# Optimization experiments

Hardware: AMD Instinct MI355X
Metric: run time of the kernel (lower is better)

The kernel has to match this reference:

```python
import jax, jax.numpy as jnp
import numpy as np

B, S = 128, 256
BERT_DIM, HID, LATENT = 768, 512, 128
V = 4096        # size of valid-token id universe (valid_ids_set ~= arange(V))
K = 100         # n_clusters
VOCAB = 30522   # bow.shape[1]


def setup_inputs() -> dict:
    key = jax.random.key(0)
    ks = jax.random.split(key, 16)
    f = jnp.float32
    s = 0.02
    return {
        "input_ids": jax.random.randint(ks[0], (B, S), 0, V),
        "valid_pos": jnp.ones((B, S), jnp.int32),
        "attention_mask": jnp.ones((B, S), jnp.int32),
        "token_embs": jax.random.normal(ks[1], (B, S, BERT_DIM), f),
        "bow": jax.random.randint(ks[2], (B, VOCAB), 0, 2).astype(f),
        "enc_w1": jax.random.normal(ks[3], (BERT_DIM, HID), f) * s,
        "enc_b1": jnp.zeros((HID,), f),
        "enc_w2": jax.random.normal(ks[4], (HID, LATENT), f) * s,
        "enc_b2": jnp.zeros((LATENT,), f),
        "dec_w1": jax.random.normal(ks[5], (LATENT, HID), f) * s,
        "dec_b1": jnp.zeros((HID,), f),
        "dec_w2": jax.random.normal(ks[6], (HID, BERT_DIM), f) * s,
        "dec_b2": jnp.zeros((BERT_DIM,), f),
        "centers": jax.random.normal(ks[7], (K, LATENT), f),
        "counts": jnp.full((K,), 50.0, f),
        "vocab_weights": jax.random.uniform(ks[8], (VOCAB,), f),
    }


def reference(input_ids, valid_pos, attention_mask, token_embs, bow,
              enc_w1, enc_b1, enc_w2, enc_b2,
              dec_w1, dec_b1, dec_w2, dec_b2,
              centers, counts, vocab_weights):
    # valid_pos is all-ones -> valid_mask selects every token; flatten [B,S,D] -> [N,D]
    x = token_embs.reshape(-1, BERT_DIM)
    # AutoEncoder: encode, L2-normalize latent, decode
    h = jax.nn.relu(x @ enc_w1 + enc_b1)
    z = h @ enc_w2 + enc_b2
    z = z / jnp.linalg.norm(z, axis=-1, keepdims=True)          # latent_embs [N,LATENT]
    rec = jax.nn.relu(z @ dec_w1 + dec_b1) @ dec_w2 + dec_b2    # bert_embs_rec [N,768]
    # segment mean over unique token ids (valid_ids_set == arange(V))
    ids = input_ids.reshape(-1)
    seg_sum = jax.ops.segment_sum(z, ids, num_segments=V)
    freq = jax.ops.segment_sum(jnp.ones_like(ids, jnp.float32), ids, num_segments=V)
    avg = seg_sum / jnp.maximum(freq, 1.0)[:, None]             # avg_latent_embs [V,LATENT]
    # co-occurrence matrix: trans_matrix gathers bow columns at valid ids (= first V cols)
    nz = (bow[:, :V] != 0).astype(jnp.float32)                  # [B,V]
    p_i = nz.sum(axis=0) / B
    p_ij = (nz.T @ nz) / B                                      # [V,V]
    co_matrix = p_ij / p_i[:, None] / p_i[None, :]
    # soft k-means assignment: normalized centers, matmul, softmax, argmax
    cn = centers / jnp.linalg.norm(centers, axis=-1, keepdims=True)
    probs = jax.nn.softmax(avg @ cn.T, axis=-1)                 # [V,K]
    cluster_ids = jnp.argmax(probs, axis=1)
    # sequential EMA centroid update (equivalent ordering to per-cluster python loops;
    # clusters are independent so a single scan in sample order matches the original)
    w = vocab_weights[:V]
    valid = (freq > 0).astype(jnp.float32)                      # skip ids never seen

    def step(carry, inp):
        c, cnt = carry
        xi, ki, wi, vi = inp
        new_cnt = cnt[ki] + vi
        cnt = cnt.at[ki].set(new_cnt)
        eta = jnp.where(vi > 0, wi / new_cnt, 0.0)
        c = c.at[ki].set((1.0 - eta) * c[ki] + eta * xi)
        return (c, cnt), None

    (new_centers, _), _ = jax.lax.scan(step, (centers, counts), (avg, cluster_ids, w, valid))
    return co_matrix, rec, avg, cluster_ids, new_centers
```

## Files before the change

### kernel.cpp

```cpp
#include <hip/hip_runtime.h>
#include <cstdint>

#define M_TOK 32768
#define BERT  768
#define HID   512
#define LAT   128
#define NV    4096
#define NK    100
#define VOCAB 30522
#define NB    128

typedef short short8 __attribute__((ext_vector_type(8)));
typedef float floatx4 __attribute__((ext_vector_type(4)));
typedef unsigned short u16x4 __attribute__((ext_vector_type(4)));

__device__ __forceinline__ unsigned short f2bf(float f) {
    unsigned u = __float_as_uint(f);
    unsigned r = (u + 0x7FFFu + ((u >> 16) & 1u)) >> 16;
    return (unsigned short)r;
}
__device__ __forceinline__ float bf2f(unsigned short h) {
    return __uint_as_float((unsigned)h << 16);
}

__device__ __forceinline__ void async16(const void* g, void* l) {
    __builtin_amdgcn_global_load_lds(
        (const __attribute__((address_space(1))) unsigned int*)g,
        (__attribute__((address_space(3))) unsigned int*)l, 16, 0, 0);
}

__global__ __launch_bounds__(256) void wsplit(
    const float* __restrict__ W, unsigned short* __restrict__ Wt,
    int K, int N)
{
    int j = blockIdx.x * 256 + threadIdx.x;
    int total = N * K;
    if (j >= total) return;
    int n = j / K, k = j - n * K;
    float v = W[(size_t)k * N + n];
    unsigned short h = f2bf(v);
    float r = v - bf2f(h);
    unsigned short m = f2bf(r);
    float r2 = r - bf2f(m);
    unsigned short l = f2bf(r2);
    Wt[j] = h;
    Wt[(size_t)total + j] = m;
    Wt[(size_t)2 * total + j] = l;
}

__global__ __launch_bounds__(256) void asplit(
    const float* __restrict__ A, unsigned short* __restrict__ P, int total)
{
    int j = (blockIdx.x * 256 + threadIdx.x) * 4;
    if (j >= total) return;
    float4 v4 = *(const float4*)(A + j);
    float vv[4] = {v4.x, v4.y, v4.z, v4.w};
    u16x4 h4, m4, l4;
#pragma unroll
    for (int e = 0; e < 4; ++e) {
        float v = vv[e];
        unsigned short h = f2bf(v);
        float r = v - bf2f(h);
        unsigned short m = f2bf(r);
        float r2 = r - bf2f(m);
        h4[e] = h; m4[e] = m; l4[e] = f2bf(r2);
    }
    *(u16x4*)(P + j) = h4;
    *(u16x4*)(P + (size_t)total + j) = m4;
    *(u16x4*)(P + (size_t)2 * total + j) = l4;
}

template<int NL, bool RELU, int OUT = 0>
__global__ __launch_bounds__(256) void gemm_mfma(
    const float* __restrict__ A, const unsigned short* __restrict__ Wt,
    const float* __restrict__ bias, float* __restrict__ C,
    int M, int N, int K)
{
    __shared__ unsigned short Ash[NL][128 * 32];
    __shared__ unsigned short Bsh[NL][128 * 32];

    const int tid  = threadIdx.x;
    const int lane = tid & 63;
    const int wave = tid >> 6;
    const int bm = blockIdx.y * 128;
    const int bn = blockIdx.x * 128;
    const int wm = (wave & 1) * 64;
    const int wn = (wave >> 1) * 64;

    const int ar = tid >> 3;
    const int ak = (tid & 7) * 4;
    const int br = tid >> 2;
    const int bk = (tid & 3) * 8;

    floatx4 acc[4][4];
#pragma unroll
    for (int t = 0; t < 4; ++t)
#pragma unroll
        for (int u = 0; u < 4; ++u)
            acc[t][u] = (floatx4)0.0f;

    float4 av[4];
#pragma unroll
    for (int i = 0; i < 4; ++i)
        av[i] = *(const float4*)(A + (size_t)(bm + ar + 32 * i) * K + ak);

    for (int k0 = 0; k0 < K; k0 += 32) {
        u16x4 ah[NL][4];
#pragma unroll
        for (int i = 0; i < 4; ++i) {
            float vv[4] = {av[i].x, av[i].y, av[i].z, av[i].w};
#pragma unroll
            for (int e = 0; e < 4; ++e) {
                float v = vv[e];
                unsigned short h = f2bf(v);
                float r = v - bf2f(h);
                unsigned short m = f2bf(r);
                ah[0][i][e] = h;
                ah[1][i][e] = m;
                if (NL == 3) {
                    float r2 = r - bf2f(m);
                    ah[2][i][e] = f2bf(r2);
                }
            }
        }
        __syncthreads();
#pragma unroll
        for (int l = 0; l < NL; ++l) {
            const unsigned short* wp = Wt + (size_t)l * N * K;
#pragma unroll
            for (int i = 0; i < 2; ++i)
                async16(wp + (size_t)(bn + br + 64 * i) * K + k0 + bk,
                        &Bsh[l][i * 2048 + tid * 8]);
        }
#pragma unroll
        for (int l = 0; l < NL; ++l)
#pragma unroll
            for (int i = 0; i < 4; ++i)
                *(u16x4*)&Ash[l][(ar + 32 * i) * 32 + ak] = ah[l][i];
        if (k0 + 32 < K) {
#pragma unroll
            for (int i = 0; i < 4; ++i)
                av[i] = *(const float4*)(A + (size_t)(bm + ar + 32 * i) * K + k0 + 32 + ak);
        }
        __syncthreads();

        short8 af[NL][4];
#pragma unroll
        for (int l = 0; l < NL; ++l)
#pragma unroll
            for (int t = 0; t < 4; ++t)
                af[l][t] = *(const short8*)&Ash[l][(wm + t * 16 + (lane & 15)) * 32 + (lane >> 4) * 8];

#pragma unroll
        for (int bl = 0; bl < NL; ++bl) {
            short8 bf[4];
#pragma unroll
            for (int u = 0; u < 4; ++u)
                bf[u] = *(const short8*)&Bsh[bl][(wn + u * 16 + (lane & 15)) * 32 + (lane >> 4) * 8];
#pragma unroll
            for (int al = 0; al < NL; ++al) {
                if (al + bl >= NL) continue;
#pragma unroll
                for (int t = 0; t < 4; ++t)
#pragma unroll
                    for (int u = 0; u < 4; ++u)
                        acc[t][u] = __builtin_amdgcn_mfma_f32_16x16x32_bf16(
                            af[al][t], bf[u], acc[t][u], 0, 0, 0);
            }
        }
    }

    unsigned short* P0 = (unsigned short*)C;
    unsigned short* P1 = P0 + (size_t)M * N;
#pragma unroll
    for (int t = 0; t < 4; ++t) {
        int row0 = bm + wm + t * 16 + (lane >> 4) * 4;
#pragma unroll
        for (int u = 0; u < 4; ++u) {
            int col = bn + wn + u * 16 + (lane & 15);
            float b = bias[col];
#pragma unroll
            for (int r = 0; r < 4; ++r) {
                float v = acc[t][u][r] + b;
                if (RELU) v = fmaxf(v, 0.f);
                if (OUT == 0) {
                    C[(size_t)(row0 + r) * N + col] = v;
                } else {
                    unsigned short hh = f2bf(v);
                    unsigned short mm = f2bf(v - bf2f(hh));
                    P0[(size_t)(row0 + r) * N + col] = hh;
                    P1[(size_t)(row0 + r) * N + col] = mm;
                }
            }
        }
    }
}

template<int NP, bool RELU>
__global__ __launch_bounds__(512, 2) void gemm8p(
    const unsigned short* __restrict__ Ap,
    const unsigned short* __restrict__ Bp,
    const float* __restrict__ bias, float* __restrict__ C,
    int M, int N, int K, int NT)
{
    __shared__ unsigned short As[2][256 * 64];
    __shared__ unsigned short Bs[2][256 * 64];

    const int tid  = threadIdx.x;
    const int lane = tid & 63;
    const int wid  = tid >> 6;
    const int wm   = (wid & 1) * 128;
    const int wn   = (wid >> 1) * 64;
    const int bm   = blockIdx.y * 256;
    const int bn   = blockIdx.x * 256;

    const int laneR = lane & 15;
    const int kgrp  = lane >> 4;
    const int swz   = lane & 7;
    const int slot0 = ((kgrp)     ^ swz) * 8;
    const int slot1 = ((4 + kgrp) ^ swz) * 8;
    const int abase = (wm + laneR) * 64;
    const int bbase = (wn + laneR) * 64;

    floatx4 acc[8][4];
#pragma unroll
    for (int m = 0; m < 8; ++m)
#pragma unroll
        for (int n = 0; n < 4; ++n) acc[m][n] = (floatx4)0.0f;

    auto stage = [&](int b, int T) {
        int c0 = 2 * T, c1 = 2 * T + 1;
        int ki0, j0, ki1, j1, al0, bl0, al1, bl1;
        if (NP == 6) {
            ki0 = c0 / 6; j0 = c0 - ki0 * 6;
            ki1 = c1 / 6; j1 = c1 - ki1 * 6;
            al0 = j0 < 3 ? j0 : (j0 < 5 ? j0 - 3 : 0);
            bl0 = j0 < 3 ? 0  : (j0 < 5 ? 1 : 2);
            al1 = j1 < 3 ? j1 : (j1 < 5 ? j1 - 3 : 0);
            bl1 = j1 < 3 ? 0  : (j1 < 5 ? 1 : 2);
        } else {
            ki0 = c0 / 3; j0 = c0 - ki0 * 3;
            ki1 = c1 / 3; j1 = c1 - ki1 * 3;
            al0 = (j0 == 1); bl0 = (j0 == 2);
            al1 = (j1 == 1); bl1 = (j1 == 2);
        }
        const unsigned short* A0 = Ap + (size_t)al0 * M * K + ki0 * 32;
        const unsigned short* A1 = Ap + (size_t)al1 * M * K + ki1 * 32;
        const unsigned short* B0 = Bp + (size_t)bl0 * N * K + ki0 * 32;
        const unsigned short* B1 = Bp + (size_t)bl1 * N * K + ki1 * 32;
#pragma unroll
        for (int i = 0; i < 4; ++i) {
            int s   = i * 512 + tid;
            int row = s >> 3;
            int e0  = ((s & 7) ^ (row & 7)) * 8;
            const unsigned short* src = ((e0 & 32) ? A1 : A0)
                                        + (size_t)(bm + row) * K + (e0 & 31);
            async16(src, &As[b][s * 8]);
        }
#pragma unroll
        for (int i = 0; i < 4; ++i) {
            int s   = i * 512 + tid;
            int row = s >> 3;
            int e0  = ((s & 7) ^ (row & 7)) * 8;
            const unsigned short* src = ((e0 & 32) ? B1 : B0)
                                        + (size_t)(bn + row) * K + (e0 & 31);
            async16(src, &Bs[b][s * 8]);
        }
    };

    stage(0, 0);
    stage(1, 1);

    for (int t = 0; t < NT; ++t) {
        const int cb = t & 1;
        if (t + 1 < NT) asm volatile("s_waitcnt vmcnt(8)" ::: "memory");
        else            asm volatile("s_waitcnt vmcnt(0)" ::: "memory");
        __builtin_amdgcn_s_barrier();
        asm volatile("" ::: "memory");

        const unsigned short* Ab = &As[cb][0];
        const unsigned short* Bb = &Bs[cb][0];
        short8 a0[4][2], a1[4][2], b0f[2][2], b1f[2][2];
#pragma unroll
        for (int m = 0; m < 4; ++m) {
            a0[m][0] = *(const short8*)&Ab[abase + m * 1024 + slot0];
            a0[m][1] = *(const short8*)&Ab[abase + m * 1024 + slot1];
        }
        __builtin_amdgcn_sched_barrier(0);
#pragma unroll
        for (int n = 0; n < 2; ++n) {
            b0f[n][0] = *(const short8*)&Bb[bbase + n * 1024 + slot0];
            b0f[n][1] = *(const short8*)&Bb[bbase + n * 1024 + slot1];
        }
        __builtin_amdgcn_sched_barrier(0);
#pragma unroll
        for (int n = 0; n < 2; ++n) {
            b1f[n][0] = *(const short8*)&Bb[bbase + (2 + n) * 1024 + slot0];
            b1f[n][1] = *(const short8*)&Bb[bbase + (2 + n) * 1024 + slot1];
        }
        __builtin_amdgcn_sched_barrier(0);
#pragma unroll
        for (int m = 0; m < 4; ++m) {
            a1[m][0] = *(const short8*)&Ab[abase + (4 + m) * 1024 + slot0];
            a1[m][1] = *(const short8*)&Ab[abase + (4 + m) * 1024 + slot1];
        }

        asm volatile("s_waitcnt lgkmcnt(12)" ::: "memory");
        __builtin_amdgcn_sched_barrier(0);
        __builtin_amdgcn_s_setprio(1);
#pragma unroll
        for (int m = 0; m < 4; ++m)
#pragma unroll
            for (int n = 0; n < 2; ++n)
#pragma unroll
                for (int kk = 0; kk < 2; ++kk)
                    acc[m][n] = __builtin_amdgcn_mfma_f32_16x16x32_bf16(
                        a0[m][kk], b0f[n][kk], acc[m][n], 0, 0, 0);
        __builtin_amdgcn_s_setprio(0);

        asm volatile("s_waitcnt lgkmcnt(8)" ::: "memory");
        __builtin_amdgcn_sched_barrier(0);
        __builtin_amdgcn_s_setprio(1);
#pragma unroll
        for (int m = 0; m < 4; ++m)
#pragma unroll
            for (int n = 0; n < 2; ++n)
#pragma unroll
                for (int kk = 0; kk < 2; ++kk)
                    acc[m][2 + n] = __builtin_amdgcn_mfma_f32_16x16x32_bf16(
                        a0[m][kk], b1f[n][kk], acc[m][2 + n], 0, 0, 0);
        __builtin_amdgcn_s_setprio(0);

        asm volatile("s_waitcnt lgkmcnt(0)" ::: "memory");
        __builtin_amdgcn_sched_barrier(0);
        asm volatile("" ::: "memory");
        __builtin_amdgcn_s_barrier();
        asm volatile("" ::: "memory");
        if (t + 2 < NT) stage(cb, t + 2);

        __builtin_amdgcn_s_setprio(1);
#pragma unroll
        for (int m = 0; m < 4; ++m)
#pragma unroll
            for (int n = 0; n < 2; ++n)
#pragma unroll
                for (int kk = 0; kk < 2; ++kk)
                    acc[4 + m][2 + n] = __builtin_amdgcn_mfma_f32_16x16x32_bf16(
                        a1[m][kk], b1f[n][kk], acc[4 + m][2 + n], 0, 0, 0);
#pragma unroll
        for (int m = 0; m < 4; ++m)
#pragma unroll
            for (int n = 0; n < 2; ++n)
#pragma unroll
                for (int kk = 0; kk < 2; ++kk)
                    acc[4 + m][n] = __builtin_amdgcn_mfma_f32_16x16x32_bf16(
                        a1[m][kk], b0f[n][kk], acc[4 + m][n], 0, 0, 0);
        __builtin_amdgcn_s_setprio(0);
    }

#pragma unroll
    for (int mf = 0; mf < 8; ++mf) {
        int row0 = bm + wm + mf * 16 + (lane >> 4) * 4;
#pragma unroll
        for (int nf = 0; nf < 4; ++nf) {
            int col = bn + wn + nf * 16 + (lane & 15);
            float b = bias[col];
#pragma unroll
            for (int r = 0; r < 4; ++r) {
                float v = acc[mf][nf][r] + b;
                if (RELU) v = fmaxf(v, 0.f);
                C[(size_t)(row0 + r) * N + col] = v;
            }
        }
    }
}

__global__ __launch_bounds__(64) void rownorm128(const float* __restrict__ in,
                                                 float* __restrict__ out)
{
    int row = blockIdx.x;
    int l = threadIdx.x;
    const float* p = in + (size_t)row * 128;
    float v0 = p[l], v1 = p[l + 64];
    float s = v0 * v0 + v1 * v1;
#pragma unroll
    for (int o = 32; o > 0; o >>= 1) s += __shfl_xor(s, o, 64);
    float inv = 1.0f / sqrtf(s);
    float* q = out + (size_t)row * 128;
    q[l] = v0 * inv;
    q[l + 64] = v1 * inv;
}

__global__ __launch_bounds__(128) void seg_scatter(
    const float* __restrict__ z, const int* __restrict__ ids,
    float* __restrict__ seg, float* __restrict__ freq)
{
    int row = blockIdx.x;
    int l = threadIdx.x;
    int id = ids[row];
    atomicAdd(&seg[(size_t)id * 128 + l], z[(size_t)row * 128 + l]);
    if (l == 0) atomicAdd(&freq[id], 1.0f);
}

__global__ __launch_bounds__(128) void avg_kernel(
    const float* __restrict__ seg, const float* __restrict__ freq,
    float* __restrict__ avg)
{
    int i = blockIdx.x;
    int l = threadIdx.x;
    float f = fmaxf(freq[i], 1.0f);
    avg[(size_t)i * 128 + l] = seg[(size_t)i * 128 + l] / f;
}

__global__ __launch_bounds__(128) void argmax_kernel(
    const float* __restrict__ avg, const float* __restrict__ cn,
    int* __restrict__ cids, float* __restrict__ cids_f)
{
    __shared__ float arow[128];
    __shared__ float lg[NK];
    int row = blockIdx.x;
    int t = threadIdx.x;
    arow[t] = avg[(size_t)row * 128 + t];
    __syncthreads();
    if (t < NK) {
        float d = 0.f;
        const float* c = cn + (size_t)t * 128;
#pragma unroll 8
        for (int i = 0; i < 128; ++i) d += arow[i] * c[i];
        lg[t] = d;
    }
    __syncthreads();
    if (t == 0) {
        float best = lg[0];
        int bi = 0;
        for (int k = 1; k < NK; ++k) {
            if (lg[k] > best) { best = lg[k]; bi = k; }
        }
        cids[row] = bi;
        cids_f[row] = (float)bi;
    }
}

__global__ __launch_bounds__(256) void build_masks(
    const float* __restrict__ bow, unsigned long long* __restrict__ masks,
    float* __restrict__ cnt)
{
    int j = blockIdx.x * 256 + threadIdx.x;
    if (j >= NV) return;
    unsigned long long m0 = 0, m1 = 0;
    for (int b = 0; b < 64; ++b)
        if (bow[(size_t)b * VOCAB + j] != 0.f) m0 |= 1ull << b;
    for (int b = 0; b < 64; ++b)
        if (bow[(size_t)(b + 64) * VOCAB + j] != 0.f) m1 |= 1ull << b;
    masks[2 * j] = m0;
    masks[2 * j + 1] = m1;
    cnt[j] = (float)(__popcll(m0) + __popcll(m1));
}

__global__ __launch_bounds__(256) void co_kernel(
    const unsigned long long* __restrict__ masks, const float* __restrict__ cnt,
    float* __restrict__ co)
{
    int j = blockIdx.x * 256 + threadIdx.x;
    unsigned long long m0 = masks[2 * j], m1 = masks[2 * j + 1];
    float cj = cnt[j];
    int ibase = blockIdx.y * 64;
    for (int ii = 0; ii < 64; ++ii) {
        int i = ibase + ii;
        unsigned long long a0 = masks[2 * i], a1 = masks[2 * i + 1];
        float ci = cnt[i];
        float c = (float)(__popcll(a0 & m0) + __popcll(a1 & m1));
        co[(size_t)i * NV + j] = (float)NB * c / (ci * cj);
    }
}

__global__ __launch_bounds__(128) void cluster_scan(
    const float* __restrict__ avg, const int* __restrict__ cids,
    const float* __restrict__ freq, const float* __restrict__ vw,
    const float* __restrict__ centers, const float* __restrict__ counts,
    float* __restrict__ out_centers)
{
    __shared__ int list[NV];
    __shared__ float coef[NV];
    __shared__ int tcnt[128];
    __shared__ int tot;
    __shared__ float Ptot;

    int k = blockIdx.x;
    int t = threadIdx.x;

    int base = t * (NV / 128);
    int c = 0;
    for (int s = 0; s < NV / 128; ++s) {
        int i = base + s;
        if (cids[i] == k && freq[i] > 0.f) c++;
    }
    tcnt[t] = c;
    __syncthreads();
    if (t == 0) {
        int run = 0;
        for (int x = 0; x < 128; ++x) { int v = tcnt[x]; tcnt[x] = run; run += v; }
        tot = run;
    }
    __syncthreads();
    int off = tcnt[t];
    for (int s = 0; s < NV / 128; ++s) {
        int i = base + s;
        if (cids[i] == k && freq[i] > 0.f) list[off++] = i;
    }
    __syncthreads();
    int m = tot;

    float c0 = counts[k];
    for (int j = t; j < m; j += 128)
        coef[j] = vw[list[j]] / (c0 + (float)(j + 1));
    __syncthreads();
    if (t == 0) {
        float suf = 1.f;
        for (int j = m - 1; j >= 0; --j) {
            float e = coef[j];
            coef[j] = e * suf;
            suf *= (1.f - e);
        }
        Ptot = suf;
    }
    __syncthreads();

    float accv = Ptot * centers[(size_t)k * 128 + t];
    for (int j = 0; j < m; ++j)
        accv += coef[j] * avg[(size_t)list[j] * 128 + t];
    out_centers[(size_t)k * 128 + t] = accv;
}

__global__ __launch_bounds__(64) void cn_norm(const float* __restrict__ centers,
                                              float* __restrict__ cn)
{
    int row = blockIdx.x;
    int l = threadIdx.x;
    const float* p = centers + (size_t)row * 128;
    float v0 = p[l], v1 = p[l + 64];
    float s = v0 * v0 + v1 * v1;
#pragma unroll
    for (int o = 32; o > 0; o >>= 1) s += __shfl_xor(s, o, 64);
    float inv = 1.0f / sqrtf(s);
    cn[(size_t)row * 128 + l] = v0 * inv;
    cn[(size_t)row * 128 + l + 64] = v1 * inv;
}

extern "C" void kernel_launch(void* const* d_in, const int* in_sizes, int n_in,
                              void* d_out, int out_size, void* d_ws, size_t ws_size,
                              hipStream_t stream)
{
    const int*   input_ids = (const int*)d_in[0];
    const float* token_embs = (const float*)d_in[3];
    const float* bow       = (const float*)d_in[4];
    const float* enc_w1    = (const float*)d_in[5];
    const float* enc_b1    = (const float*)d_in[6];
    const float* enc_w2    = (const float*)d_in[7];
    const float* enc_b2    = (const float*)d_in[8];
    const float* dec_w1    = (const float*)d_in[9];
    const float* dec_b1    = (const float*)d_in[10];
    const float* dec_w2    = (const float*)d_in[11];
    const float* dec_b2    = (const float*)d_in[12];
    const float* centers   = (const float*)d_in[13];
    const float* counts    = (const float*)d_in[14];
    const float* vocab_w   = (const float*)d_in[15];

    float* out = (float*)d_out;
    const size_t OFF_CO  = 0;
    const size_t OFF_REC = 16777216;
    const size_t OFF_AVG = OFF_REC + 25165824;
    const size_t OFF_CID = OFF_AVG + 524288;
    const size_t OFF_NC  = OFF_CID + 4096;

    float* h    = (float*)d_ws;
    float* z    = h + (size_t)M_TOK * HID;
    float* seg  = z + (size_t)M_TOK * LAT;
    float* freq = seg + (size_t)NV * LAT;
    float* cn   = freq + NV;
    float* cntv = cn + (size_t)NK * LAT;
    int*   cids = (int*)(cntv + NV);
    unsigned long long* masks = (unsigned long long*)(cids + NV);
    unsigned short* wt1 = (unsigned short*)(masks + 2 * NV);
    unsigned short* wt2 = wt1 + (size_t)3 * HID * BERT;
    unsigned short* wt3 = wt2 + (size_t)3 * LAT * HID;
    unsigned short* wt4 = wt3 + (size_t)3 * HID * LAT;

    unsigned short* a1p = (unsigned short*)out;

    hipMemsetAsync(seg, 0, (size_t)(NV * LAT + NV) * sizeof(float), stream);

    wsplit<<<(BERT * HID + 255) / 256, 256, 0, stream>>>(enc_w1, wt1, BERT, HID);
    wsplit<<<(HID * LAT + 255) / 256, 256, 0, stream>>>(enc_w2, wt2, HID, LAT);
    wsplit<<<(LAT * HID + 255) / 256, 256, 0, stream>>>(dec_w1, wt3, LAT, HID);
    wsplit<<<(HID * BERT + 255) / 256, 256, 0, stream>>>(dec_w2, wt4, HID, BERT);

    asplit<<<(M_TOK * BERT / 4 + 255) / 256, 256, 0, stream>>>(
        token_embs, a1p, M_TOK * BERT);

    gemm8p<6, true><<<dim3(HID / 256, M_TOK / 256), 512, 0, stream>>>(
        a1p, wt1, enc_b1, h, M_TOK, HID, BERT, 6 * BERT / 64);

    gemm_mfma<3, false><<<dim3(LAT / 128, M_TOK / 128), 256, 0, stream>>>(
        h, wt2, enc_b2, z, M_TOK, LAT, HID);
    rownorm128<<<M_TOK, 64, 0, stream>>>(z, z);

    gemm_mfma<2, true, 2><<<dim3(HID / 128, M_TOK / 128), 256, 0, stream>>>(
        z, wt3, dec_b1, h, M_TOK, HID, LAT);

    gemm8p<3, false><<<dim3(BERT / 256, M_TOK / 256), 512, 0, stream>>>(
        (const unsigned short*)h, wt4, dec_b2, out + OFF_REC,
        M_TOK, BERT, HID, 3 * HID / 64);

    seg_scatter<<<M_TOK, 128, 0, stream>>>(z, input_ids, seg, freq);
    avg_kernel<<<NV, 128, 0, stream>>>(seg, freq, out + OFF_AVG);

    cn_norm<<<NK, 64, 0, stream>>>(centers, cn);
    argmax_kernel<<<NV, 128, 0, stream>>>(out + OFF_AVG, cn, cids, out + OFF_CID);

    build_masks<<<NV / 256, 256, 0, stream>>>(bow, masks, cntv);
    co_kernel<<<dim3(NV / 256, NV / 64), 256, 0, stream>>>(masks, cntv, out + OFF_CO);

    cluster_scan<<<NK, 128, 0, stream>>>(out + OFF_AVG, cids, freq, vocab_w,
                                         centers, counts, out + OFF_NC);
}
```

Before: 782.9 us.

## Split GEMM tile staging into half-tile loads interleaved with MFMA phases

```diff
diff --git a/kernel.cpp b/kernel.cpp
--- a/kernel.cpp
+++ b/kernel.cpp
@@ -228,84 +228,67 @@
 #pragma unroll
         for (int n = 0; n < 4; ++n) acc[m][n] = (floatx4)0.0f;
 
-    auto stage = [&](int b, int T) {
-        int c0 = 2 * T, c1 = 2 * T + 1;
-        int ki0, j0, ki1, j1, al0, bl0, al1, bl1;
+    auto decode = [&](int c, int& ki, int& al, int& bl) {
         if (NP == 6) {
-            ki0 = c0 / 6; j0 = c0 - ki0 * 6;
-            ki1 = c1 / 6; j1 = c1 - ki1 * 6;
-            al0 = j0 < 3 ? j0 : (j0 < 5 ? j0 - 3 : 0);
-            bl0 = j0 < 3 ? 0  : (j0 < 5 ? 1 : 2);
-            al1 = j1 < 3 ? j1 : (j1 < 5 ? j1 - 3 : 0);
-            bl1 = j1 < 3 ? 0  : (j1 < 5 ? 1 : 2);
+            ki = c / 6; int j = c - ki * 6;
+            al = j < 3 ? j : (j < 5 ? j - 3 : 0);
+            bl = j < 3 ? 0 : (j < 5 ? 1 : 2);
         } else {
-            ki0 = c0 / 3; j0 = c0 - ki0 * 3;
-            ki1 = c1 / 3; j1 = c1 - ki1 * 3;
-            al0 = (j0 == 1); bl0 = (j0 == 2);
-            al1 = (j1 == 1); bl1 = (j1 == 2);
-        }
-        const unsigned short* A0 = Ap + (size_t)al0 * M * K + ki0 * 32;
-        const unsigned short* A1 = Ap + (size_t)al1 * M * K + ki1 * 32;
-        const unsigned short* B0 = Bp + (size_t)bl0 * N * K + ki0 * 32;
-        const unsigned short* B1 = Bp + (size_t)bl1 * N * K + ki1 * 32;
-#pragma unroll
-        for (int i = 0; i < 4; ++i) {
-            int s   = i * 512 + tid;
-            int row = s >> 3;
-            int e0  = ((s & 7) ^ (row & 7)) * 8;
-            const unsigned short* src = ((e0 & 32) ? A1 : A0)
-                                        + (size_t)(bm + row) * K + (e0 & 31);
-            async16(src, &As[b][s * 8]);
-        }
-#pragma unroll
-        for (int i = 0; i < 4; ++i) {
-            int s   = i * 512 + tid;
-            int row = s >> 3;
-            int e0  = ((s & 7) ^ (row & 7)) * 8;
-            const unsigned short* src = ((e0 & 32) ? B1 : B0)
-                                        + (size_t)(bn + row) * K + (e0 & 31);
-            async16(src, &Bs[b][s * 8]);
+            ki = c / 3; int j = c - ki * 3;
+            al = (j == 1); bl = (j == 2);
         }
     };
 
-    stage(0, 0);
-    stage(1, 1);
+    auto stageH = [&](int mat, int half, int T) {
+        int ki0, al0, bl0, ki1, al1, bl1;
+        decode(2 * T, ki0, al0, bl0);
+        decode(2 * T + 1, ki1, al1, bl1);
+        const unsigned short *base0, *base1;
+        int bro;
+        unsigned short* dst;
+        if (mat == 0) {
+            base0 = Ap + (size_t)al0 * M * K + (size_t)ki0 * 32;
+            base1 = Ap + (size_t)al1 * M * K + (size_t)ki1 * 32;
+            bro = bm; dst = &As[T & 1][0];
+        } else {
+            base0 = Bp + (size_t)bl0 * N * K + (size_t)ki0 * 32;
+            base1 = Bp + (size_t)bl1 * N * K + (size_t)ki1 * 32;
+            bro = bn; dst = &Bs[T & 1][0];
+        }
+#pragma unroll
+        for (int i = 0; i < 2; ++i) {
+            int row = half * 128 + i * 64 + (tid >> 3);
+            int e0  = ((tid & 7) ^ (row & 7)) * 8;
+            const unsigned short* src = ((e0 & 32) ? base1 : base0)
+                                        + (size_t)(bro + row) * K + (e0 & 31);
+            async16(src, dst + row * 64 + (tid & 7) * 8);
+        }
+    };
+
+    stageH(1, 0, 0); stageH(0, 0, 0); stageH(1, 1, 0); stageH(0, 1, 0);
+    stageH(1, 0, 1); stageH(0, 0, 1);
+    asm volatile("s_waitcnt vmcnt(4)" ::: "memory");
+    __builtin_amdgcn_s_barrier();
 
     for (int t = 0; t < NT; ++t) {
         const int cb = t & 1;
-        if (t + 1 < NT) asm volatile("s_waitcnt vmcnt(8)" ::: "memory");
-        else            asm volatile("s_waitcnt vmcnt(0)" ::: "memory");
-        __builtin_amdgcn_s_barrier();
-        asm volatile("" ::: "memory");
-
         const unsigned short* Ab = &As[cb][0];
         const unsigned short* Bb = &Bs[cb][0];
-        short8 a0[4][2], a1[4][2], b0f[2][2], b1f[2][2];
+        short8 af[4][2], bl_[2][2], bh_[2][2];
+
 #pragma unroll
         for (int m = 0; m < 4; ++m) {
-            a0[m][0] = *(const short8*)&Ab[abase + m * 1024 + slot0];
-            a0[m][1] = *(const short8*)&Ab[abase + m * 1024 + slot1];
-        }
-        __builtin_amdgcn_sched_barrier(0);
+            af[m][0] = *(const short8*)&Ab[abase + m * 1024 + slot0];
+            af[m][1] = *(const short8*)&Ab[abase + m * 1024 + slot1];
+        }
 #pragma unroll
         for (int n = 0; n < 2; ++n) {
-            b0f[n][0] = *(const short8*)&Bb[bbase + n * 1024 + slot0];
-            b0f[n][1] = *(const short8*)&Bb[bbase + n * 1024 + slot1];
-        }
-        __builtin_amdgcn_sched_barrier(0);
-#pragma unroll
-        for (int n = 0; n < 2; ++n) {
-            b1f[n][0] = *(const short8*)&Bb[bbase + (2 + n) * 1024 + slot0];
-            b1f[n][1] = *(const short8*)&Bb[bbase + (2 + n) * 1024 + slot1];
-        }
-        __builtin_amdgcn_sched_barrier(0);
-#pragma unroll
-        for (int m = 0; m < 4; ++m) {
-            a1[m][0] = *(const short8*)&Ab[abase + (4 + m) * 1024 + slot0];
-            a1[m][1] = *(const short8*)&Ab[abase + (4 + m) * 1024 + slot1];
-        }
-
-        asm volatile("s_waitcnt lgkmcnt(12)" ::: "memory");
+            bl_[n][0] = *(const short8*)&Bb[bbase + n * 1024 + slot0];
+            bl_[n][1] = *(const short8*)&Bb[bbase + n * 1024 + slot1];
+        }
+        if (t + 1 < NT) stageH(1, 1, t + 1);
+        __builtin_amdgcn_s_barrier();
+        asm volatile("s_waitcnt lgkmcnt(0)" ::: "memory");
         __builtin_amdgcn_sched_barrier(0);
         __builtin_amdgcn_s_setprio(1);
 #pragma unroll
@@ -315,10 +298,18 @@
 #pragma unroll
                 for (int kk = 0; kk < 2; ++kk)
                     acc[m][n] = __builtin_amdgcn_mfma_f32_16x16x32_bf16(
-                        a0[m][kk], b0f[n][kk], acc[m][n], 0, 0, 0);
+                        af[m][kk], bl_[n][kk], acc[m][n], 0, 0, 0);
         __builtin_amdgcn_s_setprio(0);
-
-        asm volatile("s_waitcnt lgkmcnt(8)" ::: "memory");
+        __builtin_amdgcn_s_barrier();
+
+#pragma unroll
+        for (int n = 0; n < 2; ++n) {
+            bh_[n][0] = *(const short8*)&Bb[bbase + (2 + n) * 1024 + slot0];
+            bh_[n][1] = *(const short8*)&Bb[bbase + (2 + n) * 1024 + slot1];
+        }
+        if (t + 1 < NT) stageH(0, 1, t + 1);
+        __builtin_amdgcn_s_barrier();
+        asm volatile("s_waitcnt lgkmcnt(0)" ::: "memory");
         __builtin_amdgcn_sched_barrier(0);
         __builtin_amdgcn_s_setprio(1);
 #pragma unroll
@@ -328,16 +319,19 @@
 #pragma unroll
                 for (int kk = 0; kk < 2; ++kk)
                     acc[m][2 + n] = __builtin_amdgcn_mfma_f32_16x16x32_bf16(
-                        a0[m][kk], b1f[n][kk], acc[m][2 + n], 0, 0, 0);
+                        af[m][kk], bh_[n][kk], acc[m][2 + n], 0, 0, 0);
         __builtin_amdgcn_s_setprio(0);
-
+        __builtin_amdgcn_s_barrier();
+
+#pragma unroll
+        for (int m = 0; m < 4; ++m) {
+            af[m][0] = *(const short8*)&Ab[abase + (4 + m) * 1024 + slot0];
+            af[m][1] = *(const short8*)&Ab[abase + (4 + m) * 1024 + slot1];
+        }
+        if (t + 2 < NT) stageH(1, 0, t + 2);
+        __builtin_amdgcn_s_barrier();
         asm volatile("s_waitcnt lgkmcnt(0)" ::: "memory");
         __builtin_amdgcn_sched_barrier(0);
-        asm volatile("" ::: "memory");
-        __builtin_amdgcn_s_barrier();
-        asm volatile("" ::: "memory");
-        if (t + 2 < NT) stage(cb, t + 2);
-
         __builtin_amdgcn_s_setprio(1);
 #pragma unroll
         for (int m = 0; m < 4; ++m)
@@ -346,7 +340,18 @@
 #pragma unroll
                 for (int kk = 0; kk < 2; ++kk)
                     acc[4 + m][2 + n] = __builtin_amdgcn_mfma_f32_16x16x32_bf16(
-                        a1[m][kk], b1f[n][kk], acc[4 + m][2 + n], 0, 0, 0);
+                        af[m][kk], bh_[n][kk], acc[4 + m][2 + n], 0, 0, 0);
+        __builtin_amdgcn_s_setprio(0);
+        __builtin_amdgcn_s_barrier();
+
+        if (t + 2 < NT) stageH(0, 0, t + 2);
+        if (t + 1 < NT) {
+            if (t + 2 < NT) asm volatile("s_waitcnt vmcnt(4)" ::: "memory");
+            else            asm volatile("s_waitcnt vmcnt(0)" ::: "memory");
+        }
+        __builtin_amdgcn_s_barrier();
+        __builtin_amdgcn_sched_barrier(0);
+        __builtin_amdgcn_s_setprio(1);
 #pragma unroll
         for (int m = 0; m < 4; ++m)
 #pragma unroll
@@ -354,8 +359,9 @@
 #pragma unroll
                 for (int kk = 0; kk < 2; ++kk)
                     acc[4 + m][n] = __builtin_amdgcn_mfma_f32_16x16x32_bf16(
-                        a1[m][kk], b0f[n][kk], acc[4 + m][n], 0, 0, 0);
+                        af[m][kk], bl_[n][kk], acc[4 + m][n], 0, 0, 0);
         __builtin_amdgcn_s_setprio(0);
+        __builtin_amdgcn_s_barrier();
     }
 
 #pragma unroll
```

Result: no change. 791.0 us (+1.0%).
